# Performance work log

Hardware: AMD Instinct MI355X
Metric: run time of the kernel (lower is better)

Reference implementation:

```python
import jax, jax.numpy as jnp
import numpy as np

N, E, B = 4096, 32768, 64
F_IN, E_FEAT, D, D3, G = 128, 64, 64, 64, 10
L = 3           # gc_count
SIG = 0.15      # prior_sig
LAMDA = 0.01    # DiffGroupNorm lambda
EPS = 1e-5      # BatchNorm eps


def setup_inputs() -> dict:
    key = jax.random.key(0)
    ks = jax.random.split(key, 24)
    u = lambda k, shape, s=0.02: jax.random.uniform(k, shape, jnp.float32, -s, s)
    return {
        "x": jax.random.normal(ks[0], (N, F_IN), jnp.float32),
        "edge_attr": jax.random.normal(ks[1], (E, E_FEAT), jnp.float32),
        "pre_W": u(ks[2], (F_IN, D)),
        "pre_b": u(ks[3], (D,)),
        "edge_w1": u(ks[4], (L, E_FEAT, D3), 0.1),
        "edge_b1": u(ks[5], (L, D3), 0.1),
        "edge_w2": u(ks[6], (L, D3, D * D), 0.05),
        "edge_b2": u(ks[7], (L, D * D), 0.05),
        "root_w": u(ks[8], (L, D, D), 0.1),
        "root_b": u(ks[9], (L, D), 0.1),
        "gru_wih": u(ks[10], (L, 3 * D, D), 0.1),
        "gru_whh": u(ks[11], (L, 3 * D, D), 0.1),
        "gru_bih": u(ks[12], (L, 3 * D), 0.1),
        "gru_bhh": u(ks[13], (L, 3 * D), 0.1),
        "gn_lin": u(ks[14], (L, D, G), 0.1),
        "gn_gamma": jnp.ones((L, G * D), jnp.float32),
        "gn_beta": jnp.zeros((L, G * D), jnp.float32),
        "post_W": u(ks[15], (D, D)),
        "post_b": u(ks[16], (D,)),
        "out_W": u(ks[17], (D, 1)),
        "out_b": u(ks[18], (1,)),
        "edge_index": jax.random.randint(ks[19], (2, E), 0, N),
        "batch": jnp.sort(jax.random.randint(ks[20], (N,), 0, B)),
    }


def _kld_det(W, b):
    # BayesLinear forward with sample=False: closed-form prior term
    logc = jnp.log(SIG * jnp.sqrt(2.0 * np.pi))
    return (0.5 * (W / SIG) ** 2 + logc).sum() + (0.5 * (b / SIG) ** 2 + logc).sum()


def _seg_mean(v, idx, num):
    s = jax.ops.segment_sum(v, idx, num_segments=num)
    c = jax.ops.segment_sum(jnp.ones((v.shape[0],), v.dtype), idx, num_segments=num)
    return s / jnp.clip(c, 1.0)[:, None]


def _gru_cell(m, h, wih, whh, bih, bhh):
    # torch GRU gate order: r, z, n
    gi = m @ wih.T + bih          # [N, 3D]
    gh = h @ whh.T + bhh
    i_r, i_z, i_n = jnp.split(gi, 3, axis=-1)
    h_r, h_z, h_n = jnp.split(gh, 3, axis=-1)
    r = jax.nn.sigmoid(i_r + h_r)
    z = jax.nn.sigmoid(i_z + h_z)
    n = jnp.tanh(i_n + r * h_n)
    return (1.0 - z) * n + z * h


def _diff_group_norm(m, lin, gamma, beta):
    # PyG DiffGroupNorm: x + lamda * sum_g s[:,g] * BN(s*x)
    s = jax.nn.softmax(m @ lin, axis=-1)           # [N, G]
    t = (s[:, :, None] * m[:, None, :]).reshape(m.shape[0], G * D)  # [N, G*D]
    mu = t.mean(axis=0)
    var = t.var(axis=0)                            # biased, as BatchNorm1d training
    tn = (t - mu) / jnp.sqrt(var + EPS) * gamma + beta
    return m + LAMDA * tn.reshape(m.shape[0], G, D).sum(axis=1)


def reference(x, edge_attr, pre_W, pre_b, edge_w1, edge_b1, edge_w2, edge_b2,
              root_w, root_b, gru_wih, gru_whh, gru_bih, gru_bhh,
              gn_lin, gn_gamma, gn_beta, post_W, post_b, out_W, out_b,
              edge_index, batch):
    src, dst = edge_index[0], edge_index[1]

    # pre FC (BayesLinear, sample=False) + relu
    out = jax.nn.relu(x @ pre_W + pre_b)
    tkl = _kld_det(pre_W, pre_b)
    prev = out
    h = out                                         # GRU hidden state

    for i in range(L):
        # edge-conditioned weights: MLP(edge_attr) -> [E, D, D]
        We = (jax.nn.relu(edge_attr @ edge_w1[i] + edge_b1[i]) @ edge_w2[i]
              + edge_b2[i]).reshape(E, D, D)
        msg = jnp.einsum('ef,efo->eo', out[src], We)        # gather + per-edge matmul
        agg = _seg_mean(msg, dst, N)                        # scatter-mean
        m = agg + out @ root_w[i] + root_b[i]               # NNConv root weight + bias
        m = _diff_group_norm(m, gn_lin[i], gn_gamma[i], gn_beta[i])
        m = jax.nn.relu(m)
        h = _gru_cell(m, h, gru_wih[i], gru_whh[i], gru_bih[i], gru_bhh[i])
        out = h + prev                                      # residual
        prev = out

    # early global_mean_pool over graphs
    pooled = _seg_mean(out, batch, B)                       # [B, D]
    p = jax.nn.relu(pooled @ post_W + post_b)
    tkl = tkl + _kld_det(post_W, post_b)
    y = p @ out_W + out_b                                   # [B, 1]
    tkl = tkl + _kld_det(out_W, out_b)
    return y.reshape(-1), tkl
```

## Files before the change

kernel.cpp:

```cpp
#include <hip/hip_runtime.h>
#include <math.h>

#define Nn 4096
#define Ee 32768
#define Bb 64
#define FINc 128
#define Dd 64
#define SIGf 0.15f
#define LAMf 0.01f
#define EPSf 1e-5f

typedef __attribute__((ext_vector_type(8))) short bf16x8;
typedef __attribute__((ext_vector_type(4))) float f32x4;

__device__ inline short f2bf(float f) {
  union { float f; unsigned u; } v; v.f = f;
  unsigned r = v.u + 0x7fffu + ((v.u >> 16) & 1u);
  return (short)(r >> 16);
}
__device__ inline bf16x8 pack8v(f32x4 a, f32x4 b) {
  bf16x8 r;
  r[0]=f2bf(a.x); r[1]=f2bf(a.y); r[2]=f2bf(a.z); r[3]=f2bf(a.w);
  r[4]=f2bf(b.x); r[5]=f2bf(b.y); r[6]=f2bf(b.z); r[7]=f2bf(b.w);
  return r;
}
__device__ inline float sigm(float x) { return 1.f / (1.f + expf(-x)); }

__global__ void k_tkl(const float* __restrict__ preW, const float* __restrict__ preb,
                      const float* __restrict__ postW, const float* __restrict__ postb,
                      const float* __restrict__ outW, const float* __restrict__ outb,
                      float* __restrict__ y) {
  int tid = threadIdx.x;
  const float logc = logf(SIGf * sqrtf(6.28318530717958647692f));
  const float c2 = 0.5f / (SIGf * SIGf);
  float acc = 0.f;
  for (int i = tid; i < FINc*Dd; i += 256) { float w = preW[i];  acc += c2*w*w + logc; }
  for (int i = tid; i < Dd; i += 256)      { float w = preb[i];  acc += c2*w*w + logc; }
  for (int i = tid; i < Dd*Dd; i += 256)   { float w = postW[i]; acc += c2*w*w + logc; }
  for (int i = tid; i < Dd; i += 256)      { float w = postb[i]; acc += c2*w*w + logc; }
  for (int i = tid; i < Dd; i += 256)      { float w = outW[i];  acc += c2*w*w + logc; }
  if (tid == 0)                            { float w = outb[0];  acc += c2*w*w + logc; }
  __shared__ float red[256];
  red[tid] = acc; __syncthreads();
  for (int s = 128; s > 0; s >>= 1) { if (tid < s) red[tid] += red[tid+s]; __syncthreads(); }
  if (tid == 0) y[Bb] = red[0];
}

__global__ void k_count(const int* __restrict__ dst, float* __restrict__ cnt) {
  int e = blockIdx.x * 256 + threadIdx.x;
  if (e < Ee) atomicAdd(&cnt[dst[e]], 1.0f);
}

__global__ void k_prep(const float* __restrict__ w1, const float* __restrict__ w2,
                       const float* __restrict__ b2, const float* __restrict__ rootw,
                       const float* __restrict__ gwih, const float* __restrict__ gwhh,
                       const float* __restrict__ preW,
                       short* __restrict__ w1T, short* __restrict__ b2T,
                       short* __restrict__ w2T, short* __restrict__ rootwT,
                       short* __restrict__ gwihB, short* __restrict__ gwhhB,
                       short* __restrict__ preWT) {
  int idx = blockIdx.x * 256 + threadIdx.x;
  if (idx < 3*64*64*64) {
    int f = idx & 63, o = (idx >> 6) & 63, h = (idx >> 12) & 63, l = idx >> 18;
    w2T[idx] = f2bf(w2[(((l*64 + h)*64 + f) << 6) + o]);
  }
  if (idx < 3*64*64) {
    int f = idx & 63, h = (idx >> 6) & 63, l = idx >> 12;
    w1T[idx] = f2bf(w1[l*4096 + f*64 + h]);
    b2T[idx] = f2bf(b2[l*4096 + f*64 + h]);
    rootwT[idx] = f2bf(rootw[l*4096 + f*64 + h]);
  }
  if (idx < 3*192*64) {
    gwihB[idx] = f2bf(gwih[idx]);
    gwhhB[idx] = f2bf(gwhh[idx]);
  }
  if (idx < 64*128) {
    int k = idx & 127, d = idx >> 7;
    preWT[idx] = f2bf(preW[k*64 + d]);
  }
}

__global__ __launch_bounds__(256) void k_pre(const float* __restrict__ x,
                                             const short* __restrict__ preWT,
                                             const float* __restrict__ preb,
                                             float* __restrict__ out, float* __restrict__ h) {
  const int tid = threadIdx.x, lane = tid & 63, wave = tid >> 6;
  const int m15 = lane & 15, kq = lane >> 4;
  const int nb = blockIdx.x * 16;
  const f32x4 zero4 = {0.f,0.f,0.f,0.f};
  const int d = wave*16 + m15;
  bf16x8 bfr[4];
  #pragma unroll
  for (int c = 0; c < 4; ++c)
    bfr[c] = *(const bf16x8*)(preWT + d*128 + c*32 + kq*8);
  const float* xp = x + (size_t)(nb + m15)*128 + kq*8;
  f32x4 p = zero4;
  #pragma unroll
  for (int c = 0; c < 4; ++c) {
    bf16x8 a = pack8v(*(const f32x4*)(xp + c*32), *(const f32x4*)(xp + c*32 + 4));
    p = __builtin_amdgcn_mfma_f32_16x16x32_bf16(a, bfr[c], p, 0, 0, 0);
  }
  float bv = preb[d];
  #pragma unroll
  for (int r = 0; r < 4; ++r) {
    int node = nb + kq*4 + r;
    float v = fmaxf(p[r] + bv, 0.f);
    out[node*64 + d] = v;
    h[node*64 + d] = v;
  }
}

#define MSG_PHASE(W0, W1, hh)                                                              \
  {                                                                                        \
    _Pragma("unroll")                                                                      \
    for (int t = 0; t < 4; ++t) {                                                          \
      f32x4 p = __builtin_amdgcn_mfma_f32_16x16x32_bf16(sfrag[t][0], W0, zero4, 0, 0, 0);  \
      p = __builtin_amdgcn_mfma_f32_16x16x32_bf16(sfrag[t][1], W1, p, 0, 0, 0);            \
      f32x4 hv = *(const f32x4*)(hidT + (hh)*132 + ehb + t*16 + kq*4);                     \
      acc[t] += hv * p;                                                                    \
    }                                                                                      \
  }
#define MSG_RELOAD(W0, W1, hh)                                                             \
  {                                                                                        \
    const short* fp_ = ((hh) < 64) ? (w2base + (size_t)(hh)*4096) : b2base;                \
    W0 = *(const bf16x8*)(fp_);                                                            \
    W1 = *(const bf16x8*)(fp_ + 32);                                                       \
  }

__global__ __launch_bounds__(512) void k_msg(
    const float* __restrict__ out, const float* __restrict__ edge_attr,
    const short* __restrict__ w1T, const float* __restrict__ b1,
    const short* __restrict__ w2T, const short* __restrict__ b2T,
    const int* __restrict__ src, const int* __restrict__ dst,
    float* __restrict__ agg) {
  __shared__ __align__(16) float hidT[64*132];
  __shared__ int srcv[128];
  __shared__ int dstv[128];

  const int tid  = threadIdx.x;
  const int lane = tid & 63;
  const int wave = tid >> 6;
  const int eh   = wave >> 2;
  const int ow   = wave & 3;
  const int m15  = lane & 15;
  const int kq   = lane >> 4;
  const int ehb  = eh*64;
  const int ebase = blockIdx.x * 128;

  if (tid < 128) { srcv[tid] = src[ebase + tid]; dstv[tid] = dst[ebase + tid]; }
  __syncthreads();

  const f32x4 zero4 = {0.f, 0.f, 0.f, 0.f};

  bf16x8 sfrag[4][2];
  #pragma unroll
  for (int t = 0; t < 4; ++t) {
    int node = srcv[ehb + t*16 + m15];
    const float* sp = out + node*64 + kq*8;
    #pragma unroll
    for (int ks = 0; ks < 2; ++ks) {
      f32x4 a = *(const f32x4*)(sp + ks*32);
      f32x4 b = *(const f32x4*)(sp + ks*32 + 4);
      sfrag[t][ks] = pack8v(a, b);
    }
  }

  {
    const short* wp = w1T + (ow*16 + m15)*64 + kq*8;
    bf16x8 bw0 = *(const bf16x8*)(wp);
    bf16x8 bw1 = *(const bf16x8*)(wp + 32);
    float b1v = b1[ow*16 + m15];
    #pragma unroll
    for (int t = 0; t < 4; ++t) {
      const float* ep = edge_attr + (size_t)(ebase + ehb + t*16 + m15)*64 + kq*8;
      bf16x8 a0 = pack8v(*(const f32x4*)(ep),      *(const f32x4*)(ep + 4));
      bf16x8 a1 = pack8v(*(const f32x4*)(ep + 32), *(const f32x4*)(ep + 36));
      f32x4 p = __builtin_amdgcn_mfma_f32_16x16x32_bf16(a0, bw0, zero4, 0, 0, 0);
      p = __builtin_amdgcn_mfma_f32_16x16x32_bf16(a1, bw1, p, 0, 0, 0);
      f32x4 v;
      v.x = fmaxf(p.x + b1v, 0.f); v.y = fmaxf(p.y + b1v, 0.f);
      v.z = fmaxf(p.z + b1v, 0.f); v.w = fmaxf(p.w + b1v, 0.f);
      *(f32x4*)(hidT + (ow*16 + m15)*132 + ehb + t*16 + kq*4) = v;
    }
  }
  __syncthreads();

  f32x4 acc[4] = {zero4, zero4, zero4, zero4};
  const short* w2base = w2T + (ow*16 + m15)*64 + kq*8;
  const short* b2base = b2T + (ow*16 + m15)*64 + kq*8;

  bf16x8 A0, A1, B0, B1, C0, C1, D0, D1;
  MSG_RELOAD(A0, A1, 0)
  MSG_RELOAD(B0, B1, 1)
  MSG_RELOAD(C0, C1, 2)
  MSG_RELOAD(D0, D1, 3)
  for (int h = 0; h < 64; h += 4) {
    MSG_PHASE(A0, A1, h)     MSG_RELOAD(A0, A1, h + 4)
    MSG_PHASE(B0, B1, h + 1) MSG_RELOAD(B0, B1, h + 5)
    MSG_PHASE(C0, C1, h + 2) MSG_RELOAD(C0, C1, h + 6)
    MSG_PHASE(D0, D1, h + 3) MSG_RELOAD(D0, D1, h + 7)
  }
  #pragma unroll
  for (int t = 0; t < 4; ++t) {
    f32x4 p = __builtin_amdgcn_mfma_f32_16x16x32_bf16(sfrag[t][0], A0, zero4, 0, 0, 0);
    p = __builtin_amdgcn_mfma_f32_16x16x32_bf16(sfrag[t][1], A1, p, 0, 0, 0);
    acc[t] += p;
  }

  const int o = ow*16 + m15;
  #pragma unroll
  for (int t = 0; t < 4; ++t) {
    #pragma unroll
    for (int r = 0; r < 4; ++r) {
      int e = ehb + t*16 + kq*4 + r;
      atomicAdd(&agg[dstv[e]*64 + o], acc[t][r]);
    }
  }
}

__global__ __launch_bounds__(256) void k_m_fused(
    const float* __restrict__ agg, const float* __restrict__ cnt,
    const float* __restrict__ out, const short* __restrict__ rootwT,
    const float* __restrict__ rootb, const float* __restrict__ gnlin,
    float* __restrict__ m, float* __restrict__ sbuf, float* __restrict__ stats) {
  __shared__ float msh[16*65];
  __shared__ float lgsh[16*12];
  __shared__ float ssh[16*16];
  const int tid = threadIdx.x, lane = tid & 63, wave = tid >> 6;
  const int m15 = lane & 15, kq = lane >> 4;
  const int nb = blockIdx.x * 16;
  const f32x4 zero4 = {0.f,0.f,0.f,0.f};
  const int d = wave*16 + m15;

  bf16x8 b0 = *(const bf16x8*)(rootwT + d*64 + kq*8);
  bf16x8 b1 = *(const bf16x8*)(rootwT + d*64 + 32 + kq*8);
  float rbv = rootb[d];
  {
    const float* sp = out + (size_t)(nb + m15)*64 + kq*8;
    bf16x8 a0 = pack8v(*(const f32x4*)(sp),      *(const f32x4*)(sp + 4));
    bf16x8 a1 = pack8v(*(const f32x4*)(sp + 32), *(const f32x4*)(sp + 36));
    f32x4 p = __builtin_amdgcn_mfma_f32_16x16x32_bf16(a0, b0, zero4, 0, 0, 0);
    p = __builtin_amdgcn_mfma_f32_16x16x32_bf16(a1, b1, p, 0, 0, 0);
    #pragma unroll
    for (int r = 0; r < 4; ++r) {
      int ln = kq*4 + r;
      int node = nb + ln;
      float mv = agg[node*64 + d] / fmaxf(cnt[node], 1.f) + rbv + p[r];
      m[node*64 + d] = mv;
      msh[ln*65 + d] = mv;
    }
  }
  __syncthreads();

  {
    int n = tid >> 4, g = tid & 15;
    if (g < 10) {
      float lg = 0.f;
      #pragma unroll 8
      for (int k = 0; k < 64; ++k) lg += msh[n*65 + k] * gnlin[k*10 + g];
      lgsh[n*12 + g] = lg;
    }
  }
  __syncthreads();
  {
    int n = tid >> 4, g = tid & 15;
    if (g < 10) {
      float mx = -1e30f;
      #pragma unroll
      for (int gg = 0; gg < 10; ++gg) mx = fmaxf(mx, lgsh[n*12 + gg]);
      float sum = 0.f;
      #pragma unroll
      for (int gg = 0; gg < 10; ++gg) sum += expf(lgsh[n*12 + gg] - mx);
      float sv = expf(lgsh[n*12 + g] - mx) / sum;
      sbuf[(nb + n)*16 + g] = sv;
      ssh[n*16 + g] = sv;
    }
  }
  __syncthreads();
  for (int c = tid; c < 640; c += 256) {
    int g = c >> 6, dd = c & 63;
    float a1 = 0.f, a2 = 0.f;
    #pragma unroll
    for (int n = 0; n < 16; ++n) {
      float t = ssh[n*16 + g] * msh[n*65 + dd];
      a1 += t; a2 += t*t;
    }
    atomicAdd(&stats[c], a1);
    atomicAdd(&stats[640 + c], a2);
  }
}

__global__ __launch_bounds__(256) void k_gru(
    const float* __restrict__ m, const float* __restrict__ sbuf,
    const float* __restrict__ stats, const float* __restrict__ gamma,
    const float* __restrict__ beta, const short* __restrict__ gwihB,
    const short* __restrict__ gwhhB, const float* __restrict__ bih,
    const float* __restrict__ bhh, float* __restrict__ h,
    float* __restrict__ out) {
  __shared__ __align__(16) float mrsh[16*68];
  __shared__ float igsh[640];
  __shared__ float Bsh[64];
  __shared__ float ssh[256];
  const int tid = threadIdx.x, lane = tid & 63, wave = tid >> 6;
  const int m15 = lane & 15, kq = lane >> 4;
  const int nb = blockIdx.x * 16;
  const f32x4 zero4 = {0.f,0.f,0.f,0.f};
  const float invN = 1.f / (float)Nn;

  if (tid < 64) {
    float bacc = 0.f;
    #pragma unroll
    for (int g = 0; g < 10; ++g) {
      int c = g*64 + tid;
      float mu = stats[c] * invN;
      float var = stats[640 + c] * invN - mu*mu;
      float ig = (1.0f / sqrtf(var + EPSf)) * gamma[c];
      igsh[c] = ig;
      bacc += beta[c] - mu * ig;
    }
    Bsh[tid] = bacc;
  }
  ssh[tid] = sbuf[nb*16 + tid];
  __syncthreads();

  for (int idx = tid; idx < 1024; idx += 256) {
    int n = idx >> 6, dd = idx & 63;
    float mv = m[(nb + n)*64 + dd];
    float SA = 0.f;
    #pragma unroll
    for (int g = 0; g < 10; ++g) SA += ssh[n*16 + g] * igsh[g*64 + dd];
    mrsh[n*68 + dd] = fmaxf(mv * (1.f + LAMf*SA) + LAMf*Bsh[dd], 0.f);
  }
  __syncthreads();

  bf16x8 mrf[2], hf[2];
  {
    const float* mp = mrsh + m15*68 + kq*8;
    const float* hp = h + (size_t)(nb + m15)*64 + kq*8;
    #pragma unroll
    for (int ks = 0; ks < 2; ++ks) {
      mrf[ks] = pack8v(*(const f32x4*)(mp + ks*32), *(const f32x4*)(mp + ks*32 + 4));
      hf[ks]  = pack8v(*(const f32x4*)(hp + ks*32), *(const f32x4*)(hp + ks*32 + 4));
    }
  }
  const int d = wave*16 + m15;
  f32x4 gi[3], gh[3];
  #pragma unroll
  for (int p = 0; p < 3; ++p) {
    int j = p*64 + d;
    bf16x8 bi0 = *(const bf16x8*)(gwihB + j*64 + kq*8);
    bf16x8 bi1 = *(const bf16x8*)(gwihB + j*64 + 32 + kq*8);
    bf16x8 bh0 = *(const bf16x8*)(gwhhB + j*64 + kq*8);
    bf16x8 bh1 = *(const bf16x8*)(gwhhB + j*64 + 32 + kq*8);
    f32x4 a = __builtin_amdgcn_mfma_f32_16x16x32_bf16(mrf[0], bi0, zero4, 0, 0, 0);
    gi[p] = __builtin_amdgcn_mfma_f32_16x16x32_bf16(mrf[1], bi1, a, 0, 0, 0);
    f32x4 b = __builtin_amdgcn_mfma_f32_16x16x32_bf16(hf[0], bh0, zero4, 0, 0, 0);
    gh[p] = __builtin_amdgcn_mfma_f32_16x16x32_bf16(hf[1], bh1, b, 0, 0, 0);
  }
  float bir = bih[d],      bhr = bhh[d];
  float biz = bih[64 + d], bhz = bhh[64 + d];
  float bin = bih[128 + d], bhn = bhh[128 + d];
  __syncthreads();
  #pragma unroll
  for (int r = 0; r < 4; ++r) {
    int node = nb + kq*4 + r;
    float rr = sigm(gi[0][r] + bir + gh[0][r] + bhr);
    float z  = sigm(gi[1][r] + biz + gh[1][r] + bhz);
    float nn = tanhf(gi[2][r] + bin + rr * (gh[2][r] + bhn));
    float hv = h[node*64 + d];
    float hn = (1.f - z) * nn + z * hv;
    h[node*64 + d] = hn;
    out[node*64 + d] = hn + out[node*64 + d];
  }
}

__global__ void k_pool(const float* __restrict__ out, const int* __restrict__ batch,
                       float* __restrict__ pooled, float* __restrict__ pcnt) {
  int idx = blockIdx.x * 256 + threadIdx.x;
  int n = idx >> 6, d = idx & 63;
  int b = batch[n];
  atomicAdd(&pooled[b*64 + d], out[idx]);
  if (d == 0) atomicAdd(&pcnt[b], 1.f);
}

__global__ void k_final(const float* __restrict__ pooled, const float* __restrict__ pcnt,
                        const float* __restrict__ postW, const float* __restrict__ postb,
                        const float* __restrict__ outW, const float* __restrict__ outb,
                        float* __restrict__ y) {
  int b = blockIdx.x, d = threadIdx.x;
  __shared__ float pl[64];
  float c = fmaxf(pcnt[b], 1.f);
  pl[d] = pooled[b*64 + d] / c;
  __syncthreads();
  float acc = postb[d];
  #pragma unroll 8
  for (int k = 0; k < 64; ++k) acc += pl[k] * postW[k*64 + d];
  acc = fmaxf(acc, 0.f);
  float v = acc * outW[d];
  #pragma unroll
  for (int off = 32; off > 0; off >>= 1) v += __shfl_down(v, off, 64);
  if (d == 0) y[b] = v + outb[0];
}

extern "C" void kernel_launch(void* const* d_in, const int* in_sizes, int n_in,
                              void* d_out, int out_size, void* d_ws, size_t ws_size,
                              hipStream_t stream) {
  (void)in_sizes; (void)n_in; (void)out_size; (void)ws_size;
  const float* x        = (const float*)d_in[0];
  const float* edge_attr= (const float*)d_in[1];
  const float* preW     = (const float*)d_in[2];
  const float* preb     = (const float*)d_in[3];
  const float* ew1      = (const float*)d_in[4];
  const float* eb1      = (const float*)d_in[5];
  const float* ew2      = (const float*)d_in[6];
  const float* eb2      = (const float*)d_in[7];
  const float* rootw    = (const float*)d_in[8];
  const float* rootb    = (const float*)d_in[9];
  const float* gwih     = (const float*)d_in[10];
  const float* gwhh     = (const float*)d_in[11];
  const float* gbih     = (const float*)d_in[12];
  const float* gbhh     = (const float*)d_in[13];
  const float* gnlin    = (const float*)d_in[14];
  const float* gngamma  = (const float*)d_in[15];
  const float* gnbeta   = (const float*)d_in[16];
  const float* postW    = (const float*)d_in[17];
  const float* postb    = (const float*)d_in[18];
  const float* outW     = (const float*)d_in[19];
  const float* outb     = (const float*)d_in[20];
  const int*   eidx     = (const int*)d_in[21];
  const int*   batch    = (const int*)d_in[22];
  const int* src = eidx;
  const int* dst = eidx + Ee;
  float* y = (float*)d_out;

  float* ws     = (float*)d_ws;
  float* out    = ws;
  float* hbuf   = out    + Nn*64;
  float* mbuf   = hbuf   + Nn*64;
  float* sbuf   = mbuf   + Nn*64;
  float* agg    = sbuf   + Nn*16;
  float* stats  = agg    + Nn*64;
  float* cnt    = stats  + 2048;
  float* pooled = cnt    + Nn;
  float* pcnt   = pooled + Nn;
  float* bfbase = pcnt   + 64;
  short* w1T    = (short*)bfbase;
  short* b2T    = w1T    + 3*4096;
  short* w2T    = b2T    + 3*4096;
  short* rootwT = w2T    + 3*262144;
  short* gwihB  = rootwT + 3*4096;
  short* gwhhB  = gwihB  + 3*12288;
  short* preWT  = gwhhB  + 3*12288;

  hipMemsetAsync(cnt, 0, (Nn + Nn + 64)*sizeof(float), stream);

  k_prep<<<3072, 256, 0, stream>>>(ew1, ew2, eb2, rootw, gwih, gwhh, preW,
                                   w1T, b2T, w2T, rootwT, gwihB, gwhhB, preWT);
  k_tkl<<<1, 256, 0, stream>>>(preW, preb, postW, postb, outW, outb, y);
  k_count<<<Ee/256, 256, 0, stream>>>(dst, cnt);
  k_pre<<<Nn/16, 256, 0, stream>>>(x, preWT, preb, out, hbuf);

  for (int i = 0; i < 3; ++i) {
    hipMemsetAsync(agg, 0, (Nn*64 + 2048)*sizeof(float), stream);
    k_msg<<<Ee/128, 512, 0, stream>>>(out, edge_attr,
                                     w1T + i*4096, eb1 + i*64,
                                     w2T + i*262144, b2T + i*4096,
                                     src, dst, agg);
    k_m_fused<<<Nn/16, 256, 0, stream>>>(agg, cnt, out, rootwT + i*4096,
                                         rootb + i*64, gnlin + i*640, mbuf, sbuf, stats);
    k_gru<<<Nn/16, 256, 0, stream>>>(mbuf, sbuf, stats, gngamma + i*640, gnbeta + i*640,
                                     gwihB + i*12288, gwhhB + i*12288,
                                     gbih + i*192, gbhh + i*192, hbuf, out);
  }

  k_pool<<<Nn*64/256, 256, 0, stream>>>(out, batch, pooled, pcnt);
  k_final<<<Bb, 64, 0, stream>>>(pooled, pcnt, postW, postb, outW, outb, y);
}
```

Measured before the change: 360.7 us.

## Stage edge-MLP W2 slices into swizzled LDS via async global_load_lds double buffering

The per-edge weight slices of W2 (with b2 appended as slice 64) are now converted into an XOR-swizzled layout and streamed through a double-buffered LDS tile using direct global-to-LDS loads. All waves share one cooperative copy instead of each fetching its own fragments from global memory, and the next pair of slices loads while MFMAs consume the current pair. This costs a block barrier per two slices and 32KB of extra LDS, and it adds a min-blocks launch bound that may limit registers.

```diff
diff --git a/kernel.cpp b/kernel.cpp
--- a/kernel.cpp
+++ b/kernel.cpp
@@ -10,6 +10,8 @@
 #define LAMf 0.01f
 #define EPSf 1e-5f
 
+#define W2L 266240
+
 typedef __attribute__((ext_vector_type(8))) short bf16x8;
 typedef __attribute__((ext_vector_type(4))) float f32x4;
 
@@ -25,6 +27,12 @@
   return r;
 }
 __device__ inline float sigm(float x) { return 1.f / (1.f + expf(-x)); }
+
+__device__ inline void stage16(const short* g, short* l) {
+  __builtin_amdgcn_global_load_lds(
+      (const __attribute__((address_space(1))) void*)g,
+      (__attribute__((address_space(3))) void*)l, 16, 0, 0);
+}
 
 __global__ void k_tkl(const float* __restrict__ preW, const float* __restrict__ preb,
                       const float* __restrict__ postW, const float* __restrict__ postb,
@@ -55,19 +63,22 @@
                        const float* __restrict__ b2, const float* __restrict__ rootw,
                        const float* __restrict__ gwih, const float* __restrict__ gwhh,
                        const float* __restrict__ preW,
-                       short* __restrict__ w1T, short* __restrict__ b2T,
-                       short* __restrict__ w2T, short* __restrict__ rootwT,
+                       short* __restrict__ w1T, short* __restrict__ w2T,
+                       short* __restrict__ rootwT,
                        short* __restrict__ gwihB, short* __restrict__ gwhhB,
                        short* __restrict__ preWT) {
   int idx = blockIdx.x * 256 + threadIdx.x;
   if (idx < 3*64*64*64) {
-    int f = idx & 63, o = (idx >> 6) & 63, h = (idx >> 12) & 63, l = idx >> 18;
-    w2T[idx] = f2bf(w2[(((l*64 + h)*64 + f) << 6) + o]);
+    int o = idx & 63, f = (idx >> 6) & 63, h = (idx >> 12) & 63, l = idx >> 18;
+    w2T[l*W2L + h*4096 + o*64 + (f ^ ((o & 7) << 3))] = f2bf(w2[idx]);
+  }
+  if (idx < 3*4096) {
+    int o = idx & 63, f = (idx >> 6) & 63, l = idx >> 12;
+    w2T[l*W2L + 64*4096 + o*64 + (f ^ ((o & 7) << 3))] = f2bf(b2[idx]);
   }
   if (idx < 3*64*64) {
     int f = idx & 63, h = (idx >> 6) & 63, l = idx >> 12;
     w1T[idx] = f2bf(w1[l*4096 + f*64 + h]);
-    b2T[idx] = f2bf(b2[l*4096 + f*64 + h]);
     rootwT[idx] = f2bf(rootw[l*4096 + f*64 + h]);
   }
   if (idx < 3*192*64) {
@@ -110,30 +121,14 @@
   }
 }
 
-#define MSG_PHASE(W0, W1, hh)                                                              \
-  {                                                                                        \
-    _Pragma("unroll")                                                                      \
-    for (int t = 0; t < 4; ++t) {                                                          \
-      f32x4 p = __builtin_amdgcn_mfma_f32_16x16x32_bf16(sfrag[t][0], W0, zero4, 0, 0, 0);  \
-      p = __builtin_amdgcn_mfma_f32_16x16x32_bf16(sfrag[t][1], W1, p, 0, 0, 0);            \
-      f32x4 hv = *(const f32x4*)(hidT + (hh)*132 + ehb + t*16 + kq*4);                     \
-      acc[t] += hv * p;                                                                    \
-    }                                                                                      \
-  }
-#define MSG_RELOAD(W0, W1, hh)                                                             \
-  {                                                                                        \
-    const short* fp_ = ((hh) < 64) ? (w2base + (size_t)(hh)*4096) : b2base;                \
-    W0 = *(const bf16x8*)(fp_);                                                            \
-    W1 = *(const bf16x8*)(fp_ + 32);                                                       \
-  }
-
-__global__ __launch_bounds__(512) void k_msg(
+__global__ __launch_bounds__(512, 2) void k_msg(
     const float* __restrict__ out, const float* __restrict__ edge_attr,
     const short* __restrict__ w1T, const float* __restrict__ b1,
-    const short* __restrict__ w2T, const short* __restrict__ b2T,
+    const short* __restrict__ w2S,
     const int* __restrict__ src, const int* __restrict__ dst,
     float* __restrict__ agg) {
   __shared__ __align__(16) float hidT[64*132];
+  __shared__ __align__(16) short wbuf[2][8192];
   __shared__ int srcv[128];
   __shared__ int dstv[128];
 
@@ -149,6 +144,9 @@
 
   if (tid < 128) { srcv[tid] = src[ebase + tid]; dstv[tid] = dst[ebase + tid]; }
   __syncthreads();
+
+  stage16(w2S + tid*8,        &wbuf[0][wave*512]);
+  stage16(w2S + 4096 + tid*8, &wbuf[0][4096 + wave*512]);
 
   const f32x4 zero4 = {0.f, 0.f, 0.f, 0.f};
 
@@ -186,28 +184,48 @@
   __syncthreads();
 
   f32x4 acc[4] = {zero4, zero4, zero4, zero4};
-  const short* w2base = w2T + (ow*16 + m15)*64 + kq*8;
-  const short* b2base = b2T + (ow*16 + m15)*64 + kq*8;
-
-  bf16x8 A0, A1, B0, B1, C0, C1, D0, D1;
-  MSG_RELOAD(A0, A1, 0)
-  MSG_RELOAD(B0, B1, 1)
-  MSG_RELOAD(C0, C1, 2)
-  MSG_RELOAD(D0, D1, 3)
-  for (int h = 0; h < 64; h += 4) {
-    MSG_PHASE(A0, A1, h)     MSG_RELOAD(A0, A1, h + 4)
-    MSG_PHASE(B0, B1, h + 1) MSG_RELOAD(B0, B1, h + 5)
-    MSG_PHASE(C0, C1, h + 2) MSG_RELOAD(C0, C1, h + 6)
-    MSG_PHASE(D0, D1, h + 3) MSG_RELOAD(D0, D1, h + 7)
-  }
-  #pragma unroll
-  for (int t = 0; t < 4; ++t) {
-    f32x4 p = __builtin_amdgcn_mfma_f32_16x16x32_bf16(sfrag[t][0], A0, zero4, 0, 0, 0);
-    p = __builtin_amdgcn_mfma_f32_16x16x32_bf16(sfrag[t][1], A1, p, 0, 0, 0);
-    acc[t] += p;
-  }
-
   const int o = ow*16 + m15;
+  const int sw = (o & 7) << 3;
+  const int w0off = o*64 + ((kq*8) ^ sw);
+  const int w1off = o*64 + (((kq*8) + 32) ^ sw);
+
+  int cur = 0;
+  for (int h = 0; h < 64; h += 2) {
+    {
+      const short* pg = w2S + (h + 2)*4096 + tid*8;
+      short* db = &wbuf[cur ^ 1][wave*512];
+      stage16(pg, db);
+      if (h + 3 <= 64) stage16(pg + 4096, db + 4096);
+    }
+    #pragma unroll
+    for (int s = 0; s < 2; ++s) {
+      const short* B = &wbuf[cur][s*4096];
+      bf16x8 W0 = *(const bf16x8*)(B + w0off);
+      bf16x8 W1 = *(const bf16x8*)(B + w1off);
+      const float* hp = hidT + (h + s)*132 + ehb;
+      #pragma unroll
+      for (int t = 0; t < 4; ++t) {
+        f32x4 p = __builtin_amdgcn_mfma_f32_16x16x32_bf16(sfrag[t][0], W0, zero4, 0, 0, 0);
+        p = __builtin_amdgcn_mfma_f32_16x16x32_bf16(sfrag[t][1], W1, p, 0, 0, 0);
+        f32x4 hv = *(const f32x4*)(hp + t*16 + kq*4);
+        acc[t] += hv * p;
+      }
+    }
+    __syncthreads();
+    cur ^= 1;
+  }
+  {
+    const short* B = &wbuf[cur][0];
+    bf16x8 W0 = *(const bf16x8*)(B + w0off);
+    bf16x8 W1 = *(const bf16x8*)(B + w1off);
+    #pragma unroll
+    for (int t = 0; t < 4; ++t) {
+      f32x4 p = __builtin_amdgcn_mfma_f32_16x16x32_bf16(sfrag[t][0], W0, zero4, 0, 0, 0);
+      p = __builtin_amdgcn_mfma_f32_16x16x32_bf16(sfrag[t][1], W1, p, 0, 0, 0);
+      acc[t] += p;
+    }
+  }
+
   #pragma unroll
   for (int t = 0; t < 4; ++t) {
     #pragma unroll
@@ -445,9 +463,8 @@
   float* pcnt   = pooled + Nn;
   float* bfbase = pcnt   + 64;
   short* w1T    = (short*)bfbase;
-  short* b2T    = w1T    + 3*4096;
-  short* w2T    = b2T    + 3*4096;
-  short* rootwT = w2T    + 3*262144;
+  short* w2T    = w1T    + 3*4096;
+  short* rootwT = w2T    + 3*W2L;
   short* gwihB  = rootwT + 3*4096;
   short* gwhhB  = gwihB  + 3*12288;
   short* preWT  = gwhhB  + 3*12288;
@@ -455,7 +472,7 @@
   hipMemsetAsync(cnt, 0, (Nn + Nn + 64)*sizeof(float), stream);
 
   k_prep<<<3072, 256, 0, stream>>>(ew1, ew2, eb2, rootw, gwih, gwhh, preW,
-                                   w1T, b2T, w2T, rootwT, gwihB, gwhhB, preWT);
+                                   w1T, w2T, rootwT, gwihB, gwhhB, preWT);
   k_tkl<<<1, 256, 0, stream>>>(preW, preb, postW, postb, outW, outb, y);
   k_count<<<Ee/256, 256, 0, stream>>>(dst, cnt);
   k_pre<<<Nn/16, 256, 0, stream>>>(x, preWT, preb, out, hbuf);
@@ -464,7 +481,7 @@
     hipMemsetAsync(agg, 0, (Nn*64 + 2048)*sizeof(float), stream);
     k_msg<<<Ee/128, 512, 0, stream>>>(out, edge_attr,
                                      w1T + i*4096, eb1 + i*64,
-                                     w2T + i*262144, b2T + i*4096,
+                                     w2T + i*W2L,
                                      src, dst, agg);
     k_m_fused<<<Nn/16, 256, 0, stream>>>(agg, cnt, out, rootwT + i*4096,
                                          rootb + i*64, gnlin + i*640, mbuf, sbuf, stats);
```

After: 1.299 ms. 3.6x slower.

## Split message kernel across hidden-dim slices and fuse pooling into GRU

Applied to the files above, without the earlier changes.

Each k_msg block now handles a 16-wide slice of the 64-dim edge-MLP hidden layer, with four blocks per edge tile. This cuts shared memory and per-block work, quadruples the grid and raises occupancy. The cost is recomputing the source gathers and issuing four times as many scatter atomics into agg. Separately, global mean pooling is folded into the last GRU launch, which removes one kernel launch and one re-read of out.

```diff
diff --git a/kernel.cpp b/kernel.cpp
--- a/kernel.cpp
+++ b/kernel.cpp
@@ -110,30 +110,13 @@
   }
 }
 
-#define MSG_PHASE(W0, W1, hh)                                                              \
-  {                                                                                        \
-    _Pragma("unroll")                                                                      \
-    for (int t = 0; t < 4; ++t) {                                                          \
-      f32x4 p = __builtin_amdgcn_mfma_f32_16x16x32_bf16(sfrag[t][0], W0, zero4, 0, 0, 0);  \
-      p = __builtin_amdgcn_mfma_f32_16x16x32_bf16(sfrag[t][1], W1, p, 0, 0, 0);            \
-      f32x4 hv = *(const f32x4*)(hidT + (hh)*132 + ehb + t*16 + kq*4);                     \
-      acc[t] += hv * p;                                                                    \
-    }                                                                                      \
-  }
-#define MSG_RELOAD(W0, W1, hh)                                                             \
-  {                                                                                        \
-    const short* fp_ = ((hh) < 64) ? (w2base + (size_t)(hh)*4096) : b2base;                \
-    W0 = *(const bf16x8*)(fp_);                                                            \
-    W1 = *(const bf16x8*)(fp_ + 32);                                                       \
-  }
-
-__global__ __launch_bounds__(512) void k_msg(
+__global__ __launch_bounds__(512, 8) void k_msg(
     const float* __restrict__ out, const float* __restrict__ edge_attr,
     const short* __restrict__ w1T, const float* __restrict__ b1,
     const short* __restrict__ w2T, const short* __restrict__ b2T,
     const int* __restrict__ src, const int* __restrict__ dst,
     float* __restrict__ agg) {
-  __shared__ __align__(16) float hidT[64*132];
+  __shared__ __align__(16) float hidT[16*132];
   __shared__ int srcv[128];
   __shared__ int dstv[128];
 
@@ -145,7 +128,10 @@
   const int m15  = lane & 15;
   const int kq   = lane >> 4;
   const int ehb  = eh*64;
-  const int ebase = blockIdx.x * 128;
+  const int ebi  = blockIdx.x & 255;
+  const int hs   = blockIdx.x >> 8;
+  const int h0   = hs*16;
+  const int ebase = ebi * 128;
 
   if (tid < 128) { srcv[tid] = src[ebase + tid]; dstv[tid] = dst[ebase + tid]; }
   __syncthreads();
@@ -166,48 +152,52 @@
   }
 
   {
-    const short* wp = w1T + (ow*16 + m15)*64 + kq*8;
+    const short* wp = w1T + (h0 + m15)*64 + kq*8;
     bf16x8 bw0 = *(const bf16x8*)(wp);
     bf16x8 bw1 = *(const bf16x8*)(wp + 32);
-    float b1v = b1[ow*16 + m15];
+    float b1v = b1[h0 + m15];
+    const float* ep = edge_attr + (size_t)(ebase + ehb + ow*16 + m15)*64 + kq*8;
+    bf16x8 a0 = pack8v(*(const f32x4*)(ep),      *(const f32x4*)(ep + 4));
+    bf16x8 a1 = pack8v(*(const f32x4*)(ep + 32), *(const f32x4*)(ep + 36));
+    f32x4 p = __builtin_amdgcn_mfma_f32_16x16x32_bf16(a0, bw0, zero4, 0, 0, 0);
+    p = __builtin_amdgcn_mfma_f32_16x16x32_bf16(a1, bw1, p, 0, 0, 0);
+    f32x4 v;
+    v.x = fmaxf(p.x + b1v, 0.f); v.y = fmaxf(p.y + b1v, 0.f);
+    v.z = fmaxf(p.z + b1v, 0.f); v.w = fmaxf(p.w + b1v, 0.f);
+    *(f32x4*)(hidT + m15*132 + ehb + ow*16 + kq*4) = v;
+  }
+  __syncthreads();
+
+  f32x4 acc[4] = {zero4, zero4, zero4, zero4};
+  const int o = ow*16 + m15;
+  const int w0off = o*64 + kq*8;
+
+  for (int hl = 0; hl < 16; ++hl) {
+    const short* B = w2T + (size_t)(h0 + hl)*4096 + w0off;
+    bf16x8 W0 = *(const bf16x8*)(B);
+    bf16x8 W1 = *(const bf16x8*)(B + 32);
+    const float* hp = hidT + hl*132 + ehb;
     #pragma unroll
     for (int t = 0; t < 4; ++t) {
-      const float* ep = edge_attr + (size_t)(ebase + ehb + t*16 + m15)*64 + kq*8;
-      bf16x8 a0 = pack8v(*(const f32x4*)(ep),      *(const f32x4*)(ep + 4));
-      bf16x8 a1 = pack8v(*(const f32x4*)(ep + 32), *(const f32x4*)(ep + 36));
-      f32x4 p = __builtin_amdgcn_mfma_f32_16x16x32_bf16(a0, bw0, zero4, 0, 0, 0);
-      p = __builtin_amdgcn_mfma_f32_16x16x32_bf16(a1, bw1, p, 0, 0, 0);
-      f32x4 v;
-      v.x = fmaxf(p.x + b1v, 0.f); v.y = fmaxf(p.y + b1v, 0.f);
-      v.z = fmaxf(p.z + b1v, 0.f); v.w = fmaxf(p.w + b1v, 0.f);
-      *(f32x4*)(hidT + (ow*16 + m15)*132 + ehb + t*16 + kq*4) = v;
-    }
-  }
-  __syncthreads();
-
-  f32x4 acc[4] = {zero4, zero4, zero4, zero4};
-  const short* w2base = w2T + (ow*16 + m15)*64 + kq*8;
-  const short* b2base = b2T + (ow*16 + m15)*64 + kq*8;
-
-  bf16x8 A0, A1, B0, B1, C0, C1, D0, D1;
-  MSG_RELOAD(A0, A1, 0)
-  MSG_RELOAD(B0, B1, 1)
-  MSG_RELOAD(C0, C1, 2)
-  MSG_RELOAD(D0, D1, 3)
-  for (int h = 0; h < 64; h += 4) {
-    MSG_PHASE(A0, A1, h)     MSG_RELOAD(A0, A1, h + 4)
-    MSG_PHASE(B0, B1, h + 1) MSG_RELOAD(B0, B1, h + 5)
-    MSG_PHASE(C0, C1, h + 2) MSG_RELOAD(C0, C1, h + 6)
-    MSG_PHASE(D0, D1, h + 3) MSG_RELOAD(D0, D1, h + 7)
-  }
-  #pragma unroll
-  for (int t = 0; t < 4; ++t) {
-    f32x4 p = __builtin_amdgcn_mfma_f32_16x16x32_bf16(sfrag[t][0], A0, zero4, 0, 0, 0);
-    p = __builtin_amdgcn_mfma_f32_16x16x32_bf16(sfrag[t][1], A1, p, 0, 0, 0);
-    acc[t] += p;
-  }
-
-  const int o = ow*16 + m15;
+      f32x4 p = __builtin_amdgcn_mfma_f32_16x16x32_bf16(sfrag[t][0], W0, zero4, 0, 0, 0);
+      p = __builtin_amdgcn_mfma_f32_16x16x32_bf16(sfrag[t][1], W1, p, 0, 0, 0);
+      f32x4 hv = *(const f32x4*)(hp + t*16 + kq*4);
+      acc[t] += hv * p;
+    }
+  }
+
+  if (hs == 0) {
+    const short* Bp = b2T + w0off;
+    bf16x8 W0 = *(const bf16x8*)(Bp);
+    bf16x8 W1 = *(const bf16x8*)(Bp + 32);
+    #pragma unroll
+    for (int t = 0; t < 4; ++t) {
+      f32x4 p = __builtin_amdgcn_mfma_f32_16x16x32_bf16(sfrag[t][0], W0, zero4, 0, 0, 0);
+      p = __builtin_amdgcn_mfma_f32_16x16x32_bf16(sfrag[t][1], W1, p, 0, 0, 0);
+      acc[t] += p;
+    }
+  }
+
   #pragma unroll
   for (int t = 0; t < 4; ++t) {
     #pragma unroll
@@ -296,7 +286,9 @@
     const float* __restrict__ beta, const short* __restrict__ gwihB,
     const short* __restrict__ gwhhB, const float* __restrict__ bih,
     const float* __restrict__ bhh, float* __restrict__ h,
-    float* __restrict__ out) {
+    float* __restrict__ out,
+    const int* __restrict__ batch, float* __restrict__ pooled,
+    float* __restrict__ pcnt, int doPool) {
   __shared__ __align__(16) float mrsh[16*68];
   __shared__ float igsh[640];
   __shared__ float Bsh[64];
@@ -370,17 +362,14 @@
     float hv = h[node*64 + d];
     float hn = (1.f - z) * nn + z * hv;
     h[node*64 + d] = hn;
-    out[node*64 + d] = hn + out[node*64 + d];
-  }
-}
-
-__global__ void k_pool(const float* __restrict__ out, const int* __restrict__ batch,
-                       float* __restrict__ pooled, float* __restrict__ pcnt) {
-  int idx = blockIdx.x * 256 + threadIdx.x;
-  int n = idx >> 6, d = idx & 63;
-  int b = batch[n];
-  atomicAdd(&pooled[b*64 + d], out[idx]);
-  if (d == 0) atomicAdd(&pcnt[b], 1.f);
+    float ov = hn + out[node*64 + d];
+    out[node*64 + d] = ov;
+    if (doPool) {
+      int b = batch[node];
+      atomicAdd(&pooled[b*64 + d], ov);
+      if (d == 0) atomicAdd(&pcnt[b], 1.f);
+    }
+  }
 }
 
 __global__ void k_final(const float* __restrict__ pooled, const float* __restrict__ pcnt,
@@ -462,7 +451,7 @@
 
   for (int i = 0; i < 3; ++i) {
     hipMemsetAsync(agg, 0, (Nn*64 + 2048)*sizeof(float), stream);
-    k_msg<<<Ee/128, 512, 0, stream>>>(out, edge_attr,
+    k_msg<<<(Ee/128)*4, 512, 0, stream>>>(out, edge_attr,
                                      w1T + i*4096, eb1 + i*64,
                                      w2T + i*262144, b2T + i*4096,
                                      src, dst, agg);
@@ -470,9 +459,9 @@
                                          rootb + i*64, gnlin + i*640, mbuf, sbuf, stats);
     k_gru<<<Nn/16, 256, 0, stream>>>(mbuf, sbuf, stats, gngamma + i*640, gnbeta + i*640,
                                      gwihB + i*12288, gwhhB + i*12288,
-                                     gbih + i*192, gbhh + i*192, hbuf, out);
-  }
-
-  k_pool<<<Nn*64/256, 256, 0, stream>>>(out, batch, pooled, pcnt);
+                                     gbih + i*192, gbhh + i*192, hbuf, out,
+                                     batch, pooled, pcnt, (i == 2) ? 1 : 0);
+  }
+
   k_final<<<Bb, 64, 0, stream>>>(pooled, pcnt, postW, postb, outW, outb, y);
 }
```

New measurement: 666.6 us. 84.8% more time.
